# Kernel tuning notes

Hardware: AMD Instinct MI355X
Metric: run time of the kernel (lower is better)

## Reference

```python
import jax, jax.numpy as jnp
import numpy as np

N_SPK = 8      # MAX_NO_OF_SPEAKERS
N_LAYERS = 2


def setup_inputs() -> dict:
    key = jax.random.key(0)
    B, S, H = 8, 1024, 512  # batch, seq_len, input_size==hidden_size==output_size
    k = jax.random.split(key, 6)
    x = jax.random.normal(k[0], (B, S, H), dtype=jnp.float32)
    speakers = jax.random.randint(k[1], (B, S), 0, N_SPK, dtype=jnp.int32)
    scale = 1.0 / np.sqrt(H).astype(np.float32)
    # per-speaker, per-layer GRU params (torch nn.GRU layout: gates [r,z,n])
    Wi = jax.random.uniform(k[2], (N_SPK, N_LAYERS, 3 * H, H), minval=-scale, maxval=scale, dtype=jnp.float32)
    Wh = jax.random.uniform(k[3], (N_SPK, N_LAYERS, 3 * H, H), minval=-scale, maxval=scale, dtype=jnp.float32)
    bi = jax.random.uniform(k[4], (N_SPK, N_LAYERS, 3 * H), minval=-scale, maxval=scale, dtype=jnp.float32)
    bh = jax.random.uniform(k[5], (N_SPK, N_LAYERS, 3 * H), minval=-scale, maxval=scale, dtype=jnp.float32)
    return {"x": x, "speakers": speakers, "Wi": Wi, "Wh": Wh, "bi": bi, "bh": bh}


def _gru_cell(x_t, h, Wi_l, Wh_l, bi_l, bh_l):
    # torch GRU cell: r,z,n gates
    gi = x_t @ Wi_l.T + bi_l          # [B, 3H]
    gh = h @ Wh_l.T + bh_l            # [B, 3H]
    ir, iz, i_n = jnp.split(gi, 3, axis=-1)
    hr, hz, h_n = jnp.split(gh, 3, axis=-1)
    r = jax.nn.sigmoid(ir + hr)
    z = jax.nn.sigmoid(iz + hz)
    n = jnp.tanh(i_n + r * h_n)
    return (1.0 - z) * n + z * h


def _forward(x, speakers, Wi, Wh, bi, bh):
    B, S, H = x.shape
    x_sb = jnp.swapaxes(x, 0, 1)              # [S, B, H]
    total = jnp.zeros((S, B, H), x.dtype)
    for sp in range(N_SPK):
        # masked-GRU equivalence: gathering speaker sp's utterances, running a
        # GRU, and scattering back == running over the full sequence while
        # freezing hidden state (and emitting 0) at non-sp timesteps.
        mask_sb = (speakers == sp).T          # [S, B]
        Wi_s, Wh_s, bi_s, bh_s = Wi[sp], Wh[sp], bi[sp], bh[sp]

        def step(h, xm):
            x_t, m_t = xm                     # [B,H], [B]
            m = m_t[:, None]
            inp = x_t
            new_h = []
            for l in range(N_LAYERS):
                hl = _gru_cell(inp, h[l], Wi_s[l], Wh_s[l], bi_s[l], bh_s[l])
                hl = jnp.where(m, hl, h[l])   # carry hidden across masked steps
                new_h.append(hl)
                inp = hl
            return jnp.stack(new_h), jnp.where(m, inp, 0.0)

        h0 = jnp.zeros((N_LAYERS, B, H), x.dtype)
        _, outs = jax.lax.scan(step, h0, (x_sb, mask_sb))  # outs: [S, B, H]
        total = total + outs                  # masks disjoint across speakers
    return jnp.swapaxes(total, 0, 1)          # [B, S, H]


def reference(x, speakers, Wi, Wh, bi, bh):
    return _forward(x, speakers, Wi, Wh, bi, bh)
```

## Files before the change

### kernel.cpp

```cpp
#include <hip/hip_runtime.h>
#include <cstdint>
#include <cstddef>

#define SS 1024
#define HH 512
#define G3 1536

typedef _Float16 half8 __attribute__((ext_vector_type(8)));
typedef float f32x4 __attribute__((ext_vector_type(4)));

static constexpr unsigned OFF_TLIST = 0;
static constexpr unsigned OFF_LEN   = 262144;
static constexpr unsigned OFF_META  = 262400;
static constexpr unsigned OFF_H0    = 262656;
static constexpr unsigned OFF_H1    = OFF_H0 + 262144;
static constexpr unsigned WS_NEED   = OFF_H1 + 262144;

__device__ __forceinline__ half8 cvt8(const float* p) {
  float4 u = *(const float4*)p;
  float4 v = *(const float4*)(p + 4);
  half8 h;
  h[0]=(_Float16)u.x; h[1]=(_Float16)u.y; h[2]=(_Float16)u.z; h[3]=(_Float16)u.w;
  h[4]=(_Float16)v.x; h[5]=(_Float16)v.y; h[6]=(_Float16)v.z; h[7]=(_Float16)v.w;
  return h;
}

__device__ __forceinline__ half8 pack8(uint4 a, uint4 b) {
  union { unsigned u[4]; half8 h; } r;
  r.u[0] = __builtin_amdgcn_perm(a.y, a.x, 0x05040100);
  r.u[1] = __builtin_amdgcn_perm(a.w, a.z, 0x05040100);
  r.u[2] = __builtin_amdgcn_perm(b.y, b.x, 0x05040100);
  r.u[3] = __builtin_amdgcn_perm(b.w, b.z, 0x05040100);
  return r.h;
}

__device__ __forceinline__ float sigm(float x) { return 1.f / (1.f + __expf(-x)); }

__global__ void prep_kernel(const int* __restrict__ spk, int* __restrict__ tlist,
                            int* __restrict__ len, int* __restrict__ meta) {
  __shared__ int slen[64];
  const int t = threadIdx.x;
  const int sp = t >> 3, b = t & 7;
  int cnt = 0;
  int* tl = tlist + (sp * 8 + b) * SS;
  const int4* srow = (const int4*)(spk + b * SS);
#pragma unroll 4
  for (int i = 0; i < SS / 4; ++i) {
    int4 v = srow[i];
    if (v.x == sp) tl[cnt++] = 4 * i + 0;
    if (v.y == sp) tl[cnt++] = 4 * i + 1;
    if (v.z == sp) tl[cnt++] = 4 * i + 2;
    if (v.w == sp) tl[cnt++] = 4 * i + 3;
  }
  len[t] = cnt;
  slen[t] = cnt;
  for (int i = cnt; i < SS; ++i) tl[i] = 0;
  __syncthreads();
  if (t < 8) {
    int m = 0;
    for (int i = 0; i < 8; ++i) m = max(m, slen[t * 8 + i]);
    meta[t] = m;
  }
}

__launch_bounds__(256, 1)
__global__ void gru_main(const float* __restrict__ x,
                         const float* __restrict__ Wi, const float* __restrict__ Wh,
                         const float* __restrict__ bi, const float* __restrict__ bh,
                         const int* __restrict__ tlist, const int* __restrict__ len,
                         const int* __restrict__ meta,
                         unsigned* __restrict__ h0ring, unsigned* __restrict__ h1ring,
                         float* __restrict__ out) {
  const int wg = blockIdx.x;
  const int sp = wg & 7;
  const int og = wg >> 3;
  const int j0 = og * 16;
  const int tid = threadIdx.x;
  const int w  = tid >> 6;
  const int l  = tid & 63;
  const int lr = l & 15;
  const int lg = l >> 4;
  const int b8 = lr & 7;

  __shared__ float accbuf[4][12][320];
  __shared__ unsigned hstage[2][8][516];

  const size_t WMAT = (size_t)G3 * HH;
  const float* pWi0 = Wi + (size_t)(sp * 2 + 0) * WMAT;
  const float* pWh0 = Wh + (size_t)(sp * 2 + 0) * WMAT;
  const float* pWi1 = Wi + (size_t)(sp * 2 + 1) * WMAT;
  const float* pWh1 = Wh + (size_t)(sp * 2 + 1) * WMAT;

  half8 bwi0[3][4], bwh0[3][4], bwi1[3][4], bwh1[3][4];
#pragma unroll
  for (int T = 0; T < 3; ++T) {
#pragma unroll
    for (int q = 0; q < 4; ++q) {
      const size_t row = (size_t)(T * HH + j0 + lr);
      const int k0 = lg * 8 + (w * 4 + q) * 32;
      bwi0[T][q] = cvt8(pWi0 + row * HH + k0);
      bwh0[T][q] = cvt8(pWh0 + row * HH + k0);
      bwi1[T][q] = cvt8(pWi1 + row * HH + k0);
      bwh1[T][q] = cvt8(pWh1 + row * HH + k0);
    }
  }

  const bool isA = tid < 128;
  const int u_ = isA ? tid : (tid - 128);
  const int gb = u_ >> 4;
  const int gj = u_ & 15;
  const int Lb = len[sp * 8 + gb];
  const int* tlB = tlist + (sp * 8 + gb) * SS;
  float bAi[3], bAh[3], bBi[3], bBh[3];
#pragma unroll
  for (int g = 0; g < 3; ++g) {
    const int n = g * HH + j0 + gj;
    bAi[g] = bi[(sp * 2 + 0) * G3 + n];
    bAh[g] = bh[(sp * 2 + 0) * G3 + n];
    bBi[g] = bi[(sp * 2 + 1) * G3 + n];
    bBh[g] = bh[(sp * 2 + 1) * G3 + n];
  }

  const int* tlX = tlist + (sp * 8 + b8) * SS;
  const float* xrow_base = x + (size_t)b8 * SS * HH;

  const int maxlen = meta[sp];

  float h0prev = 0.f, h1prev = 0.f;

  {
    const int tx = tlX[0];
    const float* xs = xrow_base + (size_t)tx * HH;
    half8 xf[4];
    f32x4 a0[3];
#pragma unroll
    for (int T = 0; T < 3; ++T)
#pragma unroll
      for (int e = 0; e < 4; ++e) a0[T][e] = 0.f;
#pragma unroll
    for (int q = 0; q < 4; ++q) xf[q] = cvt8(xs + lg * 8 + (w * 4 + q) * 32);
#pragma unroll
    for (int T = 0; T < 3; ++T)
#pragma unroll
      for (int q = 0; q < 4; ++q)
        a0[T] = __builtin_amdgcn_mfma_f32_16x16x32_f16(xf[q], bwi0[T][q], a0[T], 0, 0, 0);
#pragma unroll
    for (int T = 0; T < 3; ++T)
      *(f32x4*)&accbuf[w][T][lr * 20 + lg * 4] = a0[T];
  }

  for (int r = 0; r <= maxlen; ++r) {
    {
      const unsigned exp = (unsigned)r;
      const unsigned* src0 = h0ring + ((size_t)(((r - 1) & 1) * 64 + sp * 8)) * HH;
      const unsigned* src1 = h1ring + ((size_t)((r & 1) * 64 + sp * 8)) * HH;
      unsigned v0[16], v1[16];
#pragma unroll
      for (int j = 0; j < 16; ++j) {
        v0[j] = __hip_atomic_load(src0 + j * 256 + tid, __ATOMIC_RELAXED, __HIP_MEMORY_SCOPE_AGENT);
        v1[j] = __hip_atomic_load(src1 + j * 256 + tid, __ATOMIC_RELAXED, __HIP_MEMORY_SCOPE_AGENT);
      }
      unsigned iters = 0;
      while (true) {
        unsigned bad = 0;
#pragma unroll
        for (int j = 0; j < 16; ++j) {
          bad |= (v0[j] >> 16) ^ exp;
          bad |= (v1[j] >> 16) ^ exp;
        }
        if (!bad) break;
        __builtin_amdgcn_s_sleep(1);
        if (++iters > 100000000u) break;
#pragma unroll
        for (int j = 0; j < 16; ++j) {
          if ((v0[j] >> 16) != exp)
            v0[j] = __hip_atomic_load(src0 + j * 256 + tid, __ATOMIC_RELAXED, __HIP_MEMORY_SCOPE_AGENT);
          if ((v1[j] >> 16) != exp)
            v1[j] = __hip_atomic_load(src1 + j * 256 + tid, __ATOMIC_RELAXED, __HIP_MEMORY_SCOPE_AGENT);
        }
      }
#pragma unroll
      for (int j = 0; j < 16; ++j) {
        const int e = j * 256 + tid;
        hstage[0][e >> 9][e & 511] = v0[j];
        hstage[1][e >> 9][e & 511] = v1[j];
      }
    }
    __syncthreads();

    half8 hA0[4], hA1[4];
#pragma unroll
    for (int q = 0; q < 4; ++q) {
      const int k0 = lg * 8 + (w * 4 + q) * 32;
      uint4 a0 = *(const uint4*)&hstage[0][b8][k0];
      uint4 a1 = *(const uint4*)&hstage[0][b8][k0 + 4];
      uint4 c0 = *(const uint4*)&hstage[1][b8][k0];
      uint4 c1 = *(const uint4*)&hstage[1][b8][k0 + 4];
      hA0[q] = pack8(a0, a1);
      hA1[q] = pack8(c0, c1);
    }
    f32x4 acc[3][3];
#pragma unroll
    for (int Gm = 0; Gm < 3; ++Gm)
#pragma unroll
      for (int T = 0; T < 3; ++T)
#pragma unroll
        for (int e = 0; e < 4; ++e) acc[Gm][T][e] = 0.f;
#pragma unroll
    for (int T = 0; T < 3; ++T) {
#pragma unroll
      for (int q = 0; q < 4; ++q) {
        acc[0][T] = __builtin_amdgcn_mfma_f32_16x16x32_f16(hA0[q], bwh0[T][q], acc[0][T], 0, 0, 0);
        acc[1][T] = __builtin_amdgcn_mfma_f32_16x16x32_f16(hA0[q], bwi1[T][q], acc[1][T], 0, 0, 0);
        acc[2][T] = __builtin_amdgcn_mfma_f32_16x16x32_f16(hA1[q], bwh1[T][q], acc[2][T], 0, 0, 0);
      }
    }
#pragma unroll
    for (int Gm = 0; Gm < 3; ++Gm)
#pragma unroll
      for (int T = 0; T < 3; ++T)
        *(f32x4*)&accbuf[w][3 + Gm * 3 + T][lr * 20 + lg * 4] = acc[Gm][T];
    __syncthreads();

    const int ci = gj * 20 + gb;
    const unsigned tagw = ((unsigned)(r + 1)) << 16;
    if (isA) {
      if (r < Lb) {
        float giv[3], ghv[3];
#pragma unroll
        for (int g = 0; g < 3; ++g) {
          giv[g] = accbuf[0][g][ci] + accbuf[1][g][ci] + accbuf[2][g][ci] + accbuf[3][g][ci] + bAi[g];
          ghv[g] = accbuf[0][3 + g][ci] + accbuf[1][3 + g][ci] + accbuf[2][3 + g][ci] + accbuf[3][3 + g][ci] + bAh[g];
        }
        const float rr = sigm(giv[0] + ghv[0]);
        const float zz = sigm(giv[1] + ghv[1]);
        const float nn = tanhf(giv[2] + rr * ghv[2]);
        h0prev = (1.f - zz) * nn + zz * h0prev;
      }
      union { _Float16 hf; unsigned short us; } cv; cv.hf = (_Float16)h0prev;
      __hip_atomic_store(&h0ring[((size_t)((r & 1) * 64 + sp * 8 + gb)) * HH + j0 + gj],
                         tagw | (unsigned)cv.us, __ATOMIC_RELAXED, __HIP_MEMORY_SCOPE_AGENT);
    } else {
      if ((r >= 1) && (r <= Lb)) {
        float giv[3], ghv[3];
#pragma unroll
        for (int g = 0; g < 3; ++g) {
          giv[g] = accbuf[0][6 + g][ci] + accbuf[1][6 + g][ci] + accbuf[2][6 + g][ci] + accbuf[3][6 + g][ci] + bBi[g];
          ghv[g] = accbuf[0][9 + g][ci] + accbuf[1][9 + g][ci] + accbuf[2][9 + g][ci] + accbuf[3][9 + g][ci] + bBh[g];
        }
        const float rr = sigm(giv[0] + ghv[0]);
        const float zz = sigm(giv[1] + ghv[1]);
        const float nn = tanhf(giv[2] + rr * ghv[2]);
        h1prev = (1.f - zz) * nn + zz * h1prev;
        const int tcur = tlB[(r - 1) & (SS - 1)];
        out[((size_t)(gb * SS + tcur)) * HH + j0 + gj] = h1prev;
      }
      union { _Float16 hf; unsigned short us; } cv; cv.hf = (_Float16)h1prev;
      __hip_atomic_store(&h1ring[((size_t)(((r - 1) & 1) * 64 + sp * 8 + gb)) * HH + j0 + gj],
                         tagw | (unsigned)cv.us, __ATOMIC_RELAXED, __HIP_MEMORY_SCOPE_AGENT);
    }

    __syncthreads();

    {
      const int tx = tlX[(r + 1) & (SS - 1)];
      const float* xs = xrow_base + (size_t)tx * HH;
      half8 xf[4];
      f32x4 a0[3];
#pragma unroll
      for (int T = 0; T < 3; ++T)
#pragma unroll
        for (int e = 0; e < 4; ++e) a0[T][e] = 0.f;
#pragma unroll
      for (int q = 0; q < 4; ++q) xf[q] = cvt8(xs + lg * 8 + (w * 4 + q) * 32);
#pragma unroll
      for (int T = 0; T < 3; ++T)
#pragma unroll
        for (int q = 0; q < 4; ++q)
          a0[T] = __builtin_amdgcn_mfma_f32_16x16x32_f16(xf[q], bwi0[T][q], a0[T], 0, 0, 0);
#pragma unroll
      for (int T = 0; T < 3; ++T)
        *(f32x4*)&accbuf[w][T][lr * 20 + lg * 4] = a0[T];
    }
  }
}

extern "C" void kernel_launch(void* const* d_in, const int* in_sizes, int n_in,
                              void* d_out, int out_size, void* d_ws, size_t ws_size,
                              hipStream_t stream) {
  const float* x   = (const float*)d_in[0];
  const int*   spk = (const int*)d_in[1];
  const float* Wi  = (const float*)d_in[2];
  const float* Wh  = (const float*)d_in[3];
  const float* bi  = (const float*)d_in[4];
  const float* bh  = (const float*)d_in[5];
  float* out = (float*)d_out;
  char* ws = (char*)d_ws;

  int*      tlist = (int*)(ws + OFF_TLIST);
  int*      len   = (int*)(ws + OFF_LEN);
  int*      meta  = (int*)(ws + OFF_META);
  unsigned* h0r   = (unsigned*)(ws + OFF_H0);
  unsigned* h1r   = (unsigned*)(ws + OFF_H1);

  (void)in_sizes; (void)n_in; (void)out_size; (void)ws_size;

  hipMemsetAsync(ws + OFF_H0, 0, WS_NEED - OFF_H0, stream);
  prep_kernel<<<1, 64, 0, stream>>>(spk, tlist, len, meta);
  gru_main<<<256, 256, 0, stream>>>(x, Wi, Wh, bi, bh, tlist, len, meta, h0r, h1r, out);
}
```

Baseline: 723.9 us.

## Vectorize hidden-state polling with inline asm loads, mirror buffers, and double-buffered x gates

```diff
diff --git a/kernel.cpp b/kernel.cpp
--- a/kernel.cpp
+++ b/kernel.cpp
@@ -8,13 +8,16 @@
 
 typedef _Float16 half8 __attribute__((ext_vector_type(8)));
 typedef float f32x4 __attribute__((ext_vector_type(4)));
+typedef unsigned u32x4 __attribute__((ext_vector_type(4)));
 
 static constexpr unsigned OFF_TLIST = 0;
 static constexpr unsigned OFF_LEN   = 262144;
 static constexpr unsigned OFF_META  = 262400;
-static constexpr unsigned OFF_H0    = 262656;
-static constexpr unsigned OFF_H1    = OFF_H0 + 262144;
-static constexpr unsigned WS_NEED   = OFF_H1 + 262144;
+static constexpr unsigned OFF_H0UC  = 262656;
+static constexpr unsigned OFF_H1UC  = OFF_H0UC + 262144;
+static constexpr unsigned OFF_H0MIR = OFF_H1UC + 262144;
+static constexpr unsigned OFF_H1MIR = OFF_H0MIR + 262144;
+static constexpr unsigned WS_NEED   = OFF_H1MIR + 262144;
 
 __device__ __forceinline__ half8 cvt8(const float* p) {
   float4 u = *(const float4*)p;
@@ -25,16 +28,54 @@
   return h;
 }
 
-__device__ __forceinline__ half8 pack8(uint4 a, uint4 b) {
+__device__ __forceinline__ half8 pack8(u32x4 a, u32x4 b) {
   union { unsigned u[4]; half8 h; } r;
-  r.u[0] = __builtin_amdgcn_perm(a.y, a.x, 0x05040100);
-  r.u[1] = __builtin_amdgcn_perm(a.w, a.z, 0x05040100);
-  r.u[2] = __builtin_amdgcn_perm(b.y, b.x, 0x05040100);
-  r.u[3] = __builtin_amdgcn_perm(b.w, b.z, 0x05040100);
+  r.u[0] = __builtin_amdgcn_perm(a[1], a[0], 0x05040100);
+  r.u[1] = __builtin_amdgcn_perm(a[3], a[2], 0x05040100);
+  r.u[2] = __builtin_amdgcn_perm(b[1], b[0], 0x05040100);
+  r.u[3] = __builtin_amdgcn_perm(b[3], b[2], 0x05040100);
   return r.h;
 }
 
 __device__ __forceinline__ float sigm(float x) { return 1.f / (1.f + __expf(-x)); }
+
+template <bool UC>
+__device__ __forceinline__ void ld8(const unsigned* p0, const unsigned* p1,
+                                    u32x4& a0, u32x4& a1, u32x4& a2, u32x4& a3,
+                                    u32x4& b0, u32x4& b1, u32x4& b2, u32x4& b3) {
+  if constexpr (UC) {
+    asm volatile(
+      "global_load_dwordx4 %0, %8, off sc0 sc1\n\t"
+      "global_load_dwordx4 %1, %8, off offset:16 sc0 sc1\n\t"
+      "global_load_dwordx4 %2, %8, off offset:32 sc0 sc1\n\t"
+      "global_load_dwordx4 %3, %8, off offset:48 sc0 sc1\n\t"
+      "global_load_dwordx4 %4, %9, off sc0 sc1\n\t"
+      "global_load_dwordx4 %5, %9, off offset:16 sc0 sc1\n\t"
+      "global_load_dwordx4 %6, %9, off offset:32 sc0 sc1\n\t"
+      "global_load_dwordx4 %7, %9, off offset:48 sc0 sc1\n\t"
+      "s_waitcnt vmcnt(0)"
+      : "=&v"(a0), "=&v"(a1), "=&v"(a2), "=&v"(a3),
+        "=&v"(b0), "=&v"(b1), "=&v"(b2), "=&v"(b3)
+      : "v"(p0), "v"(p1)
+      : "memory");
+  } else {
+    asm volatile(
+      "global_load_dwordx4 %0, %8, off sc0\n\t"
+      "global_load_dwordx4 %1, %8, off offset:16 sc0\n\t"
+      "global_load_dwordx4 %2, %8, off offset:32 sc0\n\t"
+      "global_load_dwordx4 %3, %8, off offset:48 sc0\n\t"
+      "global_load_dwordx4 %4, %9, off sc0\n\t"
+      "global_load_dwordx4 %5, %9, off offset:16 sc0\n\t"
+      "global_load_dwordx4 %6, %9, off offset:32 sc0\n\t"
+      "global_load_dwordx4 %7, %9, off offset:48 sc0\n\t"
+      "s_waitcnt vmcnt(0)"
+      : "=&v"(a0), "=&v"(a1), "=&v"(a2), "=&v"(a3),
+        "=&v"(b0), "=&v"(b1), "=&v"(b2), "=&v"(b3)
+      : "v"(p0), "v"(p1)
+      : "memory");
+  }
+  __builtin_amdgcn_sched_barrier(0);
+}
 
 __global__ void prep_kernel(const int* __restrict__ spk, int* __restrict__ tlist,
                             int* __restrict__ len, int* __restrict__ meta) {
@@ -69,7 +110,8 @@
                          const float* __restrict__ bi, const float* __restrict__ bh,
                          const int* __restrict__ tlist, const int* __restrict__ len,
                          const int* __restrict__ meta,
-                         unsigned* __restrict__ h0ring, unsigned* __restrict__ h1ring,
+                         unsigned* __restrict__ h0uc, unsigned* __restrict__ h1uc,
+                         unsigned* __restrict__ h0mir, unsigned* __restrict__ h1mir,
                          float* __restrict__ out) {
   const int wg = blockIdx.x;
   const int sp = wg & 7;
@@ -82,8 +124,11 @@
   const int lg = l >> 4;
   const int b8 = lr & 7;
 
-  __shared__ float accbuf[4][12][320];
+  __shared__ float accbuf[4][15][320];
   __shared__ unsigned hstage[2][8][516];
+  __shared__ unsigned fbflag;
+
+  if (tid == 0) fbflag = 0;
 
   const size_t WMAT = (size_t)G3 * HH;
   const float* pWi0 = Wi + (size_t)(sp * 2 + 0) * WMAT;
@@ -128,6 +173,10 @@
 
   float h0prev = 0.f, h1prev = 0.f;
 
+  const unsigned thoff = (unsigned)tid * 16u;
+  const int srow_ = tid >> 5;
+  const int scol_ = (tid & 31) * 16;
+
   {
     const int tx = tlX[0];
     const float* xs = xrow_base + (size_t)tx * HH;
@@ -148,43 +197,46 @@
     for (int T = 0; T < 3; ++T)
       *(f32x4*)&accbuf[w][T][lr * 20 + lg * 4] = a0[T];
   }
+  __syncthreads();
 
   for (int r = 0; r <= maxlen; ++r) {
     {
       const unsigned exp = (unsigned)r;
-      const unsigned* src0 = h0ring + ((size_t)(((r - 1) & 1) * 64 + sp * 8)) * HH;
-      const unsigned* src1 = h1ring + ((size_t)((r & 1) * 64 + sp * 8)) * HH;
-      unsigned v0[16], v1[16];
-#pragma unroll
-      for (int j = 0; j < 16; ++j) {
-        v0[j] = __hip_atomic_load(src0 + j * 256 + tid, __ATOMIC_RELAXED, __HIP_MEMORY_SCOPE_AGENT);
-        v1[j] = __hip_atomic_load(src1 + j * 256 + tid, __ATOMIC_RELAXED, __HIP_MEMORY_SCOPE_AGENT);
-      }
+      const size_t sl0 = ((size_t)(((r - 1) & 1) * 64 + sp * 8)) * HH + thoff;
+      const size_t sl1 = ((size_t)((r & 1) * 64 + sp * 8)) * HH + thoff;
+      bool useUC = (fbflag != 0);
+      const unsigned* p0 = (useUC ? h0uc : h0mir) + sl0;
+      const unsigned* p1 = (useUC ? h1uc : h1mir) + sl1;
+      u32x4 a0, a1, a2, a3, c0, c1, c2, c3;
       unsigned iters = 0;
-      while (true) {
+      for (;;) {
+        if (useUC) ld8<true>(p0, p1, a0, a1, a2, a3, c0, c1, c2, c3);
+        else       ld8<false>(p0, p1, a0, a1, a2, a3, c0, c1, c2, c3);
         unsigned bad = 0;
 #pragma unroll
-        for (int j = 0; j < 16; ++j) {
-          bad |= (v0[j] >> 16) ^ exp;
-          bad |= (v1[j] >> 16) ^ exp;
+        for (int i = 0; i < 4; ++i) {
+          bad |= (a0[i] >> 16) ^ exp; bad |= (a1[i] >> 16) ^ exp;
+          bad |= (a2[i] >> 16) ^ exp; bad |= (a3[i] >> 16) ^ exp;
+          bad |= (c0[i] >> 16) ^ exp; bad |= (c1[i] >> 16) ^ exp;
+          bad |= (c2[i] >> 16) ^ exp; bad |= (c3[i] >> 16) ^ exp;
         }
         if (!bad) break;
         __builtin_amdgcn_s_sleep(1);
-        if (++iters > 100000000u) break;
-#pragma unroll
-        for (int j = 0; j < 16; ++j) {
-          if ((v0[j] >> 16) != exp)
-            v0[j] = __hip_atomic_load(src0 + j * 256 + tid, __ATOMIC_RELAXED, __HIP_MEMORY_SCOPE_AGENT);
-          if ((v1[j] >> 16) != exp)
-            v1[j] = __hip_atomic_load(src1 + j * 256 + tid, __ATOMIC_RELAXED, __HIP_MEMORY_SCOPE_AGENT);
+        ++iters;
+        if (iters == 3000u && !useUC) {
+          useUC = true; fbflag = 1u;
+          p0 = h0uc + sl0; p1 = h1uc + sl1;
         }
+        if (iters > 3000000u) break;
       }
-#pragma unroll
-      for (int j = 0; j < 16; ++j) {
-        const int e = j * 256 + tid;
-        hstage[0][e >> 9][e & 511] = v0[j];
-        hstage[1][e >> 9][e & 511] = v1[j];
-      }
+      *(u32x4*)&hstage[0][srow_][scol_ + 0]  = a0;
+      *(u32x4*)&hstage[0][srow_][scol_ + 4]  = a1;
+      *(u32x4*)&hstage[0][srow_][scol_ + 8]  = a2;
+      *(u32x4*)&hstage[0][srow_][scol_ + 12] = a3;
+      *(u32x4*)&hstage[1][srow_][scol_ + 0]  = c0;
+      *(u32x4*)&hstage[1][srow_][scol_ + 4]  = c1;
+      *(u32x4*)&hstage[1][srow_][scol_ + 8]  = c2;
+      *(u32x4*)&hstage[1][srow_][scol_ + 12] = c3;
     }
     __syncthreads();
 
@@ -192,12 +244,12 @@
 #pragma unroll
     for (int q = 0; q < 4; ++q) {
       const int k0 = lg * 8 + (w * 4 + q) * 32;
-      uint4 a0 = *(const uint4*)&hstage[0][b8][k0];
-      uint4 a1 = *(const uint4*)&hstage[0][b8][k0 + 4];
-      uint4 c0 = *(const uint4*)&hstage[1][b8][k0];
-      uint4 c1 = *(const uint4*)&hstage[1][b8][k0 + 4];
-      hA0[q] = pack8(a0, a1);
-      hA1[q] = pack8(c0, c1);
+      u32x4 t0 = *(const u32x4*)&hstage[0][b8][k0];
+      u32x4 t1 = *(const u32x4*)&hstage[0][b8][k0 + 4];
+      u32x4 t2 = *(const u32x4*)&hstage[1][b8][k0];
+      u32x4 t3 = *(const u32x4*)&hstage[1][b8][k0 + 4];
+      hA0[q] = pack8(t0, t1);
+      hA1[q] = pack8(t2, t3);
     }
     f32x4 acc[3][3];
 #pragma unroll
@@ -219,9 +271,10 @@
     for (int Gm = 0; Gm < 3; ++Gm)
 #pragma unroll
       for (int T = 0; T < 3; ++T)
-        *(f32x4*)&accbuf[w][3 + Gm * 3 + T][lr * 20 + lg * 4] = acc[Gm][T];
+        *(f32x4*)&accbuf[w][6 + Gm * 3 + T][lr * 20 + lg * 4] = acc[Gm][T];
     __syncthreads();
 
+    const int xb = 3 * (r & 1);
     const int ci = gj * 20 + gb;
     const unsigned tagw = ((unsigned)(r + 1)) << 16;
     if (isA) {
@@ -229,8 +282,10 @@
         float giv[3], ghv[3];
 #pragma unroll
         for (int g = 0; g < 3; ++g) {
-          giv[g] = accbuf[0][g][ci] + accbuf[1][g][ci] + accbuf[2][g][ci] + accbuf[3][g][ci] + bAi[g];
-          ghv[g] = accbuf[0][3 + g][ci] + accbuf[1][3 + g][ci] + accbuf[2][3 + g][ci] + accbuf[3][3 + g][ci] + bAh[g];
+          giv[g] = accbuf[0][xb + g][ci] + accbuf[1][xb + g][ci] +
+                   accbuf[2][xb + g][ci] + accbuf[3][xb + g][ci] + bAi[g];
+          ghv[g] = accbuf[0][6 + g][ci] + accbuf[1][6 + g][ci] +
+                   accbuf[2][6 + g][ci] + accbuf[3][6 + g][ci] + bAh[g];
         }
         const float rr = sigm(giv[0] + ghv[0]);
         const float zz = sigm(giv[1] + ghv[1]);
@@ -238,15 +293,19 @@
         h0prev = (1.f - zz) * nn + zz * h0prev;
       }
       union { _Float16 hf; unsigned short us; } cv; cv.hf = (_Float16)h0prev;
-      __hip_atomic_store(&h0ring[((size_t)((r & 1) * 64 + sp * 8 + gb)) * HH + j0 + gj],
-                         tagw | (unsigned)cv.us, __ATOMIC_RELAXED, __HIP_MEMORY_SCOPE_AGENT);
+      const unsigned word = tagw | (unsigned)cv.us;
+      const size_t idx = ((size_t)((r & 1) * 64 + sp * 8 + gb)) * HH + j0 + gj;
+      __hip_atomic_store(&h0uc[idx],  word, __ATOMIC_RELAXED, __HIP_MEMORY_SCOPE_AGENT);
+      __hip_atomic_store(&h0mir[idx], word, __ATOMIC_RELAXED, __HIP_MEMORY_SCOPE_WORKGROUP);
     } else {
       if ((r >= 1) && (r <= Lb)) {
         float giv[3], ghv[3];
 #pragma unroll
         for (int g = 0; g < 3; ++g) {
-          giv[g] = accbuf[0][6 + g][ci] + accbuf[1][6 + g][ci] + accbuf[2][6 + g][ci] + accbuf[3][6 + g][ci] + bBi[g];
-          ghv[g] = accbuf[0][9 + g][ci] + accbuf[1][9 + g][ci] + accbuf[2][9 + g][ci] + accbuf[3][9 + g][ci] + bBh[g];
+          giv[g] = accbuf[0][9 + g][ci] + accbuf[1][9 + g][ci] +
+                   accbuf[2][9 + g][ci] + accbuf[3][9 + g][ci] + bBi[g];
+          ghv[g] = accbuf[0][12 + g][ci] + accbuf[1][12 + g][ci] +
+                   accbuf[2][12 + g][ci] + accbuf[3][12 + g][ci] + bBh[g];
         }
         const float rr = sigm(giv[0] + ghv[0]);
         const float zz = sigm(giv[1] + ghv[1]);
@@ -256,11 +315,11 @@
         out[((size_t)(gb * SS + tcur)) * HH + j0 + gj] = h1prev;
       }
       union { _Float16 hf; unsigned short us; } cv; cv.hf = (_Float16)h1prev;
-      __hip_atomic_store(&h1ring[((size_t)(((r - 1) & 1) * 64 + sp * 8 + gb)) * HH + j0 + gj],
-                         tagw | (unsigned)cv.us, __ATOMIC_RELAXED, __HIP_MEMORY_SCOPE_AGENT);
-    }
-
-    __syncthreads();
+      const unsigned word = tagw | (unsigned)cv.us;
+      const size_t idx = ((size_t)(((r - 1) & 1) * 64 + sp * 8 + gb)) * HH + j0 + gj;
+      __hip_atomic_store(&h1uc[idx],  word, __ATOMIC_RELAXED, __HIP_MEMORY_SCOPE_AGENT);
+      __hip_atomic_store(&h1mir[idx], word, __ATOMIC_RELAXED, __HIP_MEMORY_SCOPE_WORKGROUP);
+    }
 
     {
       const int tx = tlX[(r + 1) & (SS - 1)];
@@ -280,7 +339,7 @@
           a0[T] = __builtin_amdgcn_mfma_f32_16x16x32_f16(xf[q], bwi0[T][q], a0[T], 0, 0, 0);
 #pragma unroll
       for (int T = 0; T < 3; ++T)
-        *(f32x4*)&accbuf[w][T][lr * 20 + lg * 4] = a0[T];
+        *(f32x4*)&accbuf[w][3 * ((r + 1) & 1) + T][lr * 20 + lg * 4] = a0[T];
     }
   }
 }
@@ -300,12 +359,15 @@
   int*      tlist = (int*)(ws + OFF_TLIST);
   int*      len   = (int*)(ws + OFF_LEN);
   int*      meta  = (int*)(ws + OFF_META);
-  unsigned* h0r   = (unsigned*)(ws + OFF_H0);
-  unsigned* h1r   = (unsigned*)(ws + OFF_H1);
+  unsigned* h0uc  = (unsigned*)(ws + OFF_H0UC);
+  unsigned* h1uc  = (unsigned*)(ws + OFF_H1UC);
+  unsigned* h0mir = (unsigned*)(ws + OFF_H0MIR);
+  unsigned* h1mir = (unsigned*)(ws + OFF_H1MIR);
 
   (void)in_sizes; (void)n_in; (void)out_size; (void)ws_size;
 
-  hipMemsetAsync(ws + OFF_H0, 0, WS_NEED - OFF_H0, stream);
+  hipMemsetAsync(ws + OFF_H0UC, 0, WS_NEED - OFF_H0UC, stream);
   prep_kernel<<<1, 64, 0, stream>>>(spk, tlist, len, meta);
-  gru_main<<<256, 256, 0, stream>>>(x, Wi, Wh, bi, bh, tlist, len, meta, h0r, h1r, out);
-}
+  gru_main<<<256, 256, 0, stream>>>(x, Wi, Wh, bi, bh, tlist, len, meta,
+                                    h0uc, h1uc, h0mir, h1mir, out);
+}
```

New measurement: 2.470 ms. 241% more time.
